# Optimization experiments

Hardware: AMD Instinct MI355X
Metric: run time of the kernel (lower is better)

Reference implementation:

```python
import jax, jax.numpy as jnp
import numpy as np

STRIDE = 1
PAD = 1

def setup_inputs() -> dict:
    key = jax.random.key(0)
    k1, k2 = jax.random.split(key)
    x = jax.random.normal(k1, (32, 128, 56, 56), dtype=jnp.float32)
    W = jax.random.normal(k2, (256, 128, 3, 3), dtype=jnp.float32)
    b = jnp.zeros((256,), dtype=jnp.float32)
    return {"x": x, "W": W, "b": b}

def reference(x, W, b):
    # Faithful conv2d: NCHW input, OIHW weight, stride 1, pad 1, plus bias.
    out = jax.lax.conv_general_dilated(
        x, W,
        window_strides=(STRIDE, STRIDE),
        padding=((PAD, PAD), (PAD, PAD)),
        dimension_numbers=("NCHW", "OIHW", "NCHW"),
    )
    return out + b[None, :, None, None]
```

## Files before the change

kernel.cpp:

```cpp
#include <hip/hip_runtime.h>
#include <hip/hip_bf16.h>
#include <cstdint>
#include <cstddef>

#define NB   32
#define CIN  128
#define HWP  3136
#define KOC  256
#define NRS  9
#define PROW 3364
#define GUARD 256
#define AEL  12288
#define BEL  8192

typedef __attribute__((ext_vector_type(8))) short  short8;
typedef __attribute__((ext_vector_type(4))) short  short4v;
typedef __attribute__((ext_vector_type(4))) float  float4v;

__device__ __forceinline__ unsigned short f2bf(float f) {
    union { float f; unsigned int u; } v; v.f = f;
    unsigned int u = v.u;
    u = u + 0x7fffu + ((u >> 16) & 1u);
    return (unsigned short)(u >> 16);
}

__global__ __launch_bounds__(256) void prep_kernel(const float* __restrict__ W,
                                                   unsigned short* __restrict__ wt2,
                                                   const float* __restrict__ x,
                                                   unsigned short* __restrict__ xt) {
    __shared__ unsigned short lds[32 * 260];
    int blk = blockIdx.x;
    int t   = threadIdx.x;

    if (blk < 1152) {
        int idx  = blk * 256 + t;
        int e    = idx & 7;
        int lr   = (idx >> 3) & 15;
        int quad = (idx >> 7) & 3;
        int i    = (idx >> 9) & 3;
        int wm   = (idx >> 11) & 1;
        int rem  = idx >> 12;
        int s    = rem % 3;
        int q    = rem / 3;
        int ot   = q & 1;
        int r    = (q >> 1) % 3;
        int ck   = q / 6;
        int rs   = r * 3 + s;
        int oc = ot * 128 + wm * 64 + i * 16 + lr;
        int c  = ck * 32 + quad * 8 + e;
        wt2[idx] = f2bf(W[((size_t)oc * CIN + c) * NRS + rs]);
        return;
    }

    if (blk >= 2816) {
        int g = (blk - 2816) * 256 + t;
        int slab = g / 228;
        int gi   = g - slab * 228;
        int row;
        if (gi < 59)       row = gi;
        else if (gi < 169) { int k = gi - 59;
                             row = 115 + 58 * (k >> 1) + (k & 1); }
        else               row = 3305 + (gi - 169);
        unsigned short* gr = xt + (size_t)slab * (PROW * 32) + (size_t)row * 32;
        short8 z = (short8)0;
        *(short8*)(gr +  0) = z;
        *(short8*)(gr +  8) = z;
        *(short8*)(gr + 16) = z;
        *(short8*)(gr + 24) = z;
        return;
    }

    int b    = blk - 1152;
    int tile = b % 13;
    int ck   = (b / 13) & 3;
    int n    = b / 52;
    int hw0  = tile * 256;
    int wv   = t >> 6;
    int lane = t & 63;

    const float* src = x + ((size_t)(n * CIN + ck * 32)) * HWP;
    #pragma unroll
    for (int pass = 0; pass < 8; ++pass) {
        int c  = pass * 4 + wv;
        int hw = hw0 + lane * 4;
        if (hw < HWP) {
            float4v v = *(const float4v*)(src + (size_t)c * HWP + hw);
            short4v s4;
            #pragma unroll
            for (int k = 0; k < 4; ++k) s4[k] = (short)f2bf(v[k]);
            *(short4v*)(&lds[c * 260 + lane * 4]) = s4;
        }
    }
    __syncthreads();

    int sub = t & 3;
    int hwl = t >> 2;
    unsigned short* dst = xt + ((size_t)(n * 4 + ck)) * PROW * 32;
    #pragma unroll
    for (int pass = 0; pass < 4; ++pass) {
        int hl = pass * 64 + hwl;
        int hw = hw0 + hl;
        if (hw < HWP) {
            short8 v;
            #pragma unroll
            for (int j = 0; j < 8; ++j)
                v[j] = (short)lds[(sub * 8 + j) * 260 + hl];
            int pr = hw + 59 + 2 * (hw / 56);
            *(short8*)(dst + (size_t)pr * 32 + sub * 8) = v;
        }
    }
}

__device__ __forceinline__ void stage_A(const unsigned short* src,
                                        unsigned short* lbase,
                                        int wv, int lane) {
    #pragma unroll
    for (int it = 0; it < 6; ++it) {
        int c0 = it * 256 + wv * 64;
        __builtin_amdgcn_global_load_lds(
            (const __attribute__((address_space(1))) void*)(src + (size_t)(c0 + lane) * 8),
            (__attribute__((address_space(3))) void*)(lbase + (size_t)c0 * 8), 16, 0, 0);
    }
}

__device__ __forceinline__ void stage_B(const unsigned short* gwin,
                                        unsigned short* lbase,
                                        int wv, int lane) {
    #pragma unroll
    for (int it = 0; it < 4; ++it) {
        int blk = it * 4 + wv;
        int s   = blk * 64 + lane;
        int r   = s >> 2;
        int q   = s & 3;
        int qs  = q ^ ((r >> 1) & 3);
        __builtin_amdgcn_global_load_lds(
            (const __attribute__((address_space(1))) void*)(gwin + r * 32 + qs * 8),
            (__attribute__((address_space(3))) void*)(lbase + (size_t)blk * 512), 16, 0, 0);
    }
}

__device__ __forceinline__ short8 ldb(const char* lb, int r, int quad) {
    int q = quad ^ ((r >> 1) & 3);
    return *(const short8*)(lb + r * 64 + q * 16);
}

__global__ __launch_bounds__(256, 2) void gemm_kernel(const unsigned short* __restrict__ xt,
                                                      const unsigned short* __restrict__ wt2,
                                                      const float* __restrict__ bias,
                                                      float* __restrict__ out) {
    __shared__ unsigned short lds[40960];

    int bx = blockIdx.x;
    int ot = bx & 1;
    int n  = (bx >> 1) & 31;
    int pt = bx >> 6;
    int p0 = pt * 128;

    int t    = threadIdx.x;
    int wv   = t >> 6;
    int lane = t & 63;
    int lr   = lane & 15;
    int quad = lane >> 4;
    int wm   = wv >> 1;
    int wn   = wv & 1;

    int prbase = p0 + 2 * (p0 / 56);

    int rb[4];
    #pragma unroll
    for (int j = 0; j < 4; ++j) {
        int hw  = p0 + wn * 64 + j * 16 + lr;
        int hwc = hw < HWP ? hw : (HWP - 1);
        rb[j] = hwc + 59 + 2 * (hwc / 56) - prbase;
    }

    const unsigned short* xb = xt + (size_t)n * 4 * PROW * 32;
    const unsigned short* wb = wt2 + ot * AEL;

    float4v acc[4][4];
    #pragma unroll
    for (int i = 0; i < 4; ++i)
        #pragma unroll
        for (int j = 0; j < 4; ++j)
            acc[i][j] = (float4v){0.f, 0.f, 0.f, 0.f};

    stage_A(wb, lds, wv, lane);
    stage_B(xb + (size_t)prbase * 32, lds + 24576, wv, lane);
    __syncthreads();

    for (int ck = 0; ck < 4; ++ck) {
        for (int r = 0; r < 3; ++r) {
            int g = ck * 3 + r;
            if (g < 11) {
                int r2  = (r == 2) ? 0 : r + 1;
                int ck2 = (r == 2) ? ck + 1 : ck;
                stage_A(wb + (size_t)ck2 * 73728 + (size_t)r2 * 24576,
                        lds + ((g + 1) & 1) * AEL, wv, lane);
            }
            if (r == 2 && ck < 3)
                stage_B(xb + (size_t)(ck + 1) * (PROW * 32) + (size_t)prbase * 32,
                        lds + 24576 + ((ck + 1) & 1) * BEL, wv, lane);

            const unsigned short* A = lds + (g & 1) * AEL + wm * 2048 + lane * 8;
            const char* lbB = (const char*)(lds + 24576 + (ck & 1) * BEL);
            int sh0 = (r - 1) * 58;

            #pragma unroll
            for (int s = 0; s < 3; ++s) {
                int shift = sh0 + s - 1;
                short8 af[4];
                #pragma unroll
                for (int i = 0; i < 4; ++i)
                    af[i] = *(const short8*)(A + s * 4096 + i * 512);
                short8 bcur = ldb(lbB, rb[0] + shift, quad);
                __builtin_amdgcn_s_setprio(1);
                #pragma unroll
                for (int j = 0; j < 4; ++j) {
                    short8 bnext;
                    if (j < 3) bnext = ldb(lbB, rb[j + 1] + shift, quad);
                    #pragma unroll
                    for (int i = 0; i < 4; ++i)
                        acc[i][j] = __builtin_amdgcn_mfma_f32_16x16x32_bf16(
                            af[i], bcur, acc[i][j], 0, 0, 0);
                    if (j < 3) bcur = bnext;
                }
                __builtin_amdgcn_s_setprio(0);
            }
            __syncthreads();
        }
    }

    float* orow = out + (size_t)n * KOC * HWP;
    #pragma unroll
    for (int i = 0; i < 4; ++i) {
        #pragma unroll
        for (int rr = 0; rr < 4; ++rr) {
            int oc = ot * 128 + wm * 64 + i * 16 + quad * 4 + rr;
            float bi = bias[oc];
            #pragma unroll
            for (int j = 0; j < 4; ++j) {
                int hw = p0 + wn * 64 + j * 16 + lr;
                if (hw < HWP)
                    orow[(size_t)oc * HWP + hw] = acc[i][j][rr] + bi;
            }
        }
    }
}

__global__ void naive_kernel(const float* __restrict__ x, const float* __restrict__ W,
                             const float* __restrict__ b, float* __restrict__ out) {
    size_t idx = (size_t)blockIdx.x * 256 + threadIdx.x;
    if (idx >= (size_t)NB * KOC * HWP) return;
    int w0 = (int)(idx % 56);
    int h0 = (int)((idx / 56) % 56);
    int k  = (int)((idx / HWP) % KOC);
    int n  = (int)(idx / ((size_t)HWP * KOC));
    float acc = b[k];
    for (int c = 0; c < CIN; ++c) {
        const float* xr = x + ((size_t)n * CIN + c) * HWP;
        const float* wr = W + ((size_t)k * CIN + c) * NRS;
        for (int r = 0; r < 3; ++r) {
            int h = h0 + r - 1;
            if ((unsigned)h >= 56u) continue;
            for (int s = 0; s < 3; ++s) {
                int w = w0 + s - 1;
                if ((unsigned)w >= 56u) continue;
                acc += xr[h * 56 + w] * wr[r * 3 + s];
            }
        }
    }
    out[idx] = acc;
}

extern "C" void kernel_launch(void* const* d_in, const int* in_sizes, int n_in,
                              void* d_out, int out_size, void* d_ws, size_t ws_size,
                              hipStream_t stream) {
    const float* x  = (const float*)d_in[0];
    const float* W  = (const float*)d_in[1];
    const float* b  = (const float*)d_in[2];
    float* out = (float*)d_out;

    const size_t wt_elems = (size_t)NRS * 4 * 2 * 2 * 4 * 4 * 16 * 8;
    const size_t xt_elems = (size_t)NB * 4 * PROW * 32 + (size_t)GUARD * 32;
    const size_t need = (wt_elems + xt_elems) * sizeof(unsigned short);

    if (ws_size < need) {
        size_t total = (size_t)NB * KOC * HWP;
        naive_kernel<<<(unsigned)((total + 255) / 256), 256, 0, stream>>>(x, W, b, out);
        return;
    }

    unsigned short* wt2 = (unsigned short*)d_ws;
    unsigned short* xt  = wt2 + wt_elems;

    prep_kernel<<<1152 + NB * 4 * 13 + 114, 256, 0, stream>>>(W, wt2, x, xt);
    gemm_kernel<<<1600, 256, 0, stream>>>(xt, wt2, b, out);
}
```

Baseline: 211.5 us.

## Load conv weights straight into registers with rotating prefetch, dropping LDS A staging

Weight fragments now go from global memory into a 12-register rotating buffer, prefetched two filter taps ahead, instead of being double-buffered through LDS. The weight repack layout changes to match. LDS drops to the two activation buffers, which allows a launch bound of 3 blocks per CU. Barriers fall from one per filter row to one per channel chunk. In exchange, global or L2 load latency now sits inside the MFMA loop, and the last prefetch reads past the end of the weight buffer.

```diff
diff --git a/kernel.cpp b/kernel.cpp
--- a/kernel.cpp
+++ b/kernel.cpp
@@ -10,7 +10,6 @@
 #define NRS  9
 #define PROW 3364
 #define GUARD 256
-#define AEL  12288
 #define BEL  8192
 
 typedef __attribute__((ext_vector_type(8))) short  short8;
@@ -37,18 +36,15 @@
         int e    = idx & 7;
         int lr   = (idx >> 3) & 15;
         int quad = (idx >> 7) & 3;
-        int i    = (idx >> 9) & 3;
-        int wm   = (idx >> 11) & 1;
-        int rem  = idx >> 12;
-        int s    = rem % 3;
-        int q    = rem / 3;
-        int ot   = q & 1;
-        int r    = (q >> 1) % 3;
-        int ck   = q / 6;
-        int rs   = r * 3 + s;
-        int oc = ot * 128 + wm * 64 + i * 16 + lr;
+        int i4   = (idx >> 9) & 3;
+        int w4   = (idx >> 11) & 3;
+        int q13  = idx >> 13;
+        int s    = q13 % 3;
+        int r    = (q13 / 3) % 3;
+        int ck   = q13 / 9;
+        int oc = w4 * 64 + i4 * 16 + lr;
         int c  = ck * 32 + quad * 8 + e;
-        wt2[idx] = f2bf(W[((size_t)oc * CIN + c) * NRS + rs]);
+        wt2[idx] = f2bf(W[((size_t)oc * CIN + c) * NRS + r * 3 + s]);
         return;
     }
 
@@ -111,18 +107,6 @@
     }
 }
 
-__device__ __forceinline__ void stage_A(const unsigned short* src,
-                                        unsigned short* lbase,
-                                        int wv, int lane) {
-    #pragma unroll
-    for (int it = 0; it < 6; ++it) {
-        int c0 = it * 256 + wv * 64;
-        __builtin_amdgcn_global_load_lds(
-            (const __attribute__((address_space(1))) void*)(src + (size_t)(c0 + lane) * 8),
-            (__attribute__((address_space(3))) void*)(lbase + (size_t)c0 * 8), 16, 0, 0);
-    }
-}
-
 __device__ __forceinline__ void stage_B(const unsigned short* gwin,
                                         unsigned short* lbase,
                                         int wv, int lane) {
@@ -144,11 +128,11 @@
     return *(const short8*)(lb + r * 64 + q * 16);
 }
 
-__global__ __launch_bounds__(256, 2) void gemm_kernel(const unsigned short* __restrict__ xt,
+__global__ __launch_bounds__(256, 3) void gemm_kernel(const unsigned short* __restrict__ xt,
                                                       const unsigned short* __restrict__ wt2,
                                                       const float* __restrict__ bias,
                                                       float* __restrict__ out) {
-    __shared__ unsigned short lds[40960];
+    __shared__ unsigned short lds[2 * BEL];
 
     int bx = blockIdx.x;
     int ot = bx & 1;
@@ -175,7 +159,7 @@
     }
 
     const unsigned short* xb = xt + (size_t)n * 4 * PROW * 32;
-    const unsigned short* wb = wt2 + ot * AEL;
+    const unsigned short* ap = wt2 + (ot * 2 + wm) * 2048 + lane * 8;
 
     float4v acc[4][4];
     #pragma unroll
@@ -184,34 +168,29 @@
         for (int j = 0; j < 4; ++j)
             acc[i][j] = (float4v){0.f, 0.f, 0.f, 0.f};
 
-    stage_A(wb, lds, wv, lane);
-    stage_B(xb + (size_t)prbase * 32, lds + 24576, wv, lane);
+    short8 af[12];
+
+    stage_B(xb + (size_t)prbase * 32, lds, wv, lane);
+    #pragma unroll
+    for (int k = 0; k < 8; ++k)
+        af[k] = *(const short8*)(ap + (size_t)(k >> 2) * 8192 + (size_t)(k & 3) * 512);
     __syncthreads();
 
     for (int ck = 0; ck < 4; ++ck) {
+        const char* lbB = (const char*)(lds + (ck & 1) * BEL);
+        #pragma unroll
         for (int r = 0; r < 3; ++r) {
-            int g = ck * 3 + r;
-            if (g < 11) {
-                int r2  = (r == 2) ? 0 : r + 1;
-                int ck2 = (r == 2) ? ck + 1 : ck;
-                stage_A(wb + (size_t)ck2 * 73728 + (size_t)r2 * 24576,
-                        lds + ((g + 1) & 1) * AEL, wv, lane);
-            }
-            if (r == 2 && ck < 3)
-                stage_B(xb + (size_t)(ck + 1) * (PROW * 32) + (size_t)prbase * 32,
-                        lds + 24576 + ((ck + 1) & 1) * BEL, wv, lane);
-
-            const unsigned short* A = lds + (g & 1) * AEL + wm * 2048 + lane * 8;
-            const char* lbB = (const char*)(lds + 24576 + (ck & 1) * BEL);
+            const unsigned short* gb = ap + (size_t)(ck * 9 + r * 3) * 8192;
             int sh0 = (r - 1) * 58;
 
             #pragma unroll
             for (int s = 0; s < 3; ++s) {
-                int shift = sh0 + s - 1;
-                short8 af[4];
+                const int db = 4 * ((s + 2) % 3);
                 #pragma unroll
                 for (int i = 0; i < 4; ++i)
-                    af[i] = *(const short8*)(A + s * 4096 + i * 512);
+                    af[db + i] = *(const short8*)(gb + (size_t)(s + 2) * 8192
+                                                     + (size_t)i * 512);
+                int shift = sh0 + s - 1;
                 short8 bcur = ldb(lbB, rb[0] + shift, quad);
                 __builtin_amdgcn_s_setprio(1);
                 #pragma unroll
@@ -221,13 +200,16 @@
                     #pragma unroll
                     for (int i = 0; i < 4; ++i)
                         acc[i][j] = __builtin_amdgcn_mfma_f32_16x16x32_bf16(
-                            af[i], bcur, acc[i][j], 0, 0, 0);
+                            af[4 * s + i], bcur, acc[i][j], 0, 0, 0);
                     if (j < 3) bcur = bnext;
                 }
                 __builtin_amdgcn_s_setprio(0);
             }
-            __syncthreads();
-        }
+        }
+        if (ck < 3)
+            stage_B(xb + (size_t)(ck + 1) * (PROW * 32) + (size_t)prbase * 32,
+                    lds + ((ck + 1) & 1) * BEL, wv, lane);
+        __syncthreads();
     }
 
     float* orow = out + (size_t)n * KOC * HWP;
```

After: 238.8 us. 1.13x slower.
